# Optimization experiments

Hardware: AMD Instinct MI355X
Metric: run time of the kernel (lower is better)

Reference implementation:

```python
import jax, jax.numpy as jnp
import numpy as np

BETA = 0.25
NUM_CODES = 1024
EMBED_DIM = 256


def setup_inputs() -> dict:
    key = jax.random.key(0)
    k1, k2 = jax.random.split(key)
    z = jax.random.normal(k1, (64, 32, 32, EMBED_DIM), dtype=jnp.float32)
    # torch init: uniform(-1/num_codes, 1/num_codes)
    codebook = jax.random.uniform(k2, (NUM_CODES, EMBED_DIM), dtype=jnp.float32,
                                  minval=-1.0 / NUM_CODES, maxval=1.0 / NUM_CODES)
    return {"z": z, "codebook": codebook}


def reference(z, codebook):
    shape = z.shape
    z_flat = z.reshape(-1, EMBED_DIM)  # [N, D]
    # squared-distance matrix: ||z||^2 + ||c||^2 - 2 z c^T  -> [N, K]
    d = (jnp.sum(z_flat * z_flat, axis=1, keepdims=True)
         + jnp.sum(codebook * codebook, axis=1)
         - 2.0 * jnp.einsum('nd,kd->nk', z_flat, codebook))
    codes = jnp.argmin(d, axis=1)              # [N] int
    quantized = codebook[codes]                # [N, D] gather
    sg = jax.lax.stop_gradient
    cb_loss = jnp.mean((quantized - sg(z_flat)) ** 2)
    cmt_loss = jnp.mean((z_flat - sg(quantized)) ** 2)
    vq_loss = cb_loss + BETA * cmt_loss
    # straight-through estimator
    out = z_flat + sg(quantized - z_flat)
    return out.reshape(shape), codes.reshape(shape[:-1]), vq_loss
```

## Files before the change

### kernel.cpp

```cpp
#include <hip/hip_runtime.h>


#define N_PTS    65536
#define K_CODES  1024
#define DIM      256
#define MARGIN   1.5e-4f
#define WSKIP    4096

#define OUT_VALS  16777216
#define OUT_CODES 65536

typedef __attribute__((ext_vector_type(8))) short short8v;
typedef __attribute__((ext_vector_type(8))) _Float16 half8v;
typedef __attribute__((ext_vector_type(4))) float float4v;

__device__ __forceinline__ int perm_idx(int r, int k) {
  return ((((r >> 4) * 8 + (k >> 5)) * 4 + ((k >> 3) & 3)) * 128) + (r & 15) * 8 + (k & 7);
}

__device__ __forceinline__ short f2h_bits(float x) {
  union { _Float16 h; short s; } u;
  u.h = (_Float16)x;
  return u.s;
}

__device__ __forceinline__ void gload16(const void* g, void* l) {
  __builtin_amdgcn_global_load_lds(
      (const __attribute__((address_space(1))) unsigned*)g,
      (__attribute__((address_space(3))) unsigned*)l, 16, 0, 0);
}

__global__ void prep_cb_kernel(const float* __restrict__ cb,
                               short* __restrict__ cbh_perm,
                               float* __restrict__ Bf,
                               unsigned long long* __restrict__ scratch,
                               unsigned long long* __restrict__ ws0) {
  const int gid = blockIdx.x * 256 + threadIdx.x;
  scratch[gid] = ~0ull;
  if (gid < 512) ws0[gid] = 0ull;
  int r    = blockIdx.x * 4 + (threadIdx.x >> 6);
  int lane = threadIdx.x & 63;
  const float4 v = *(const float4*)(cb + (size_t)r * DIM + lane * 4);
  double s = (double)v.x * v.x + (double)v.y * v.y
           + (double)v.z * v.z + (double)v.w * v.w;
#pragma unroll
  for (int off = 32; off > 0; off >>= 1) s += __shfl_down(s, off);
  if (lane == 0) Bf[r] = (float)s;
  short4 h = make_short4(f2h_bits(v.x * 1024.0f), f2h_bits(v.y * 1024.0f),
                         f2h_bits(v.z * 1024.0f), f2h_bits(v.w * 1024.0f));
  *(short4*)(cbh_perm + perm_idx(r, lane * 4)) = h;
}

__global__ __launch_bounds__(512, 4) void argmin_mfma_kernel(
    const float* __restrict__ z, const float* __restrict__ cb,
    const short* __restrict__ cbh_perm,
    const float* __restrict__ Bf, float* __restrict__ outq,
    float* __restrict__ codes_out,
    int* __restrict__ cnt2, int* __restrict__ cntf,
    unsigned* __restrict__ flag2, int* __restrict__ flagf,
    float* __restrict__ bv2a, float* __restrict__ bvfa,
    double* __restrict__ loss_slots) {
  __shared__ __align__(16) short lbuf[2][2][4096];
  __shared__ float mv1[128][2], mv2[128][2], mv3[128][2];
  __shared__ int   mk1[128][2], mk2[128][2];
  __shared__ float mz[128];
  __shared__ int   scodes[128];
  __shared__ double wls[2];
  const int t    = threadIdx.x;
  const int w    = t >> 6;
  const int l    = t & 63;
  const int quad = l >> 4;
  const int lr   = l & 15;
  const int wp   = w >> 1;
  const int h    = w & 1;
  const int m0   = blockIdx.x * 128;
  const int pbase = m0 + wp * 32;

  {
    const char* src = (const char*)cbh_perm + (size_t)(h * 32) * 8192 + wp * 2048;
    char* dst = (char*)&lbuf[h][0][0] + wp * 2048;
    gload16(src + l * 16, dst + l * 16);
    gload16(src + 1024 + l * 16, dst + 1024 + l * 16);
  }

  half8v ah[2][8];
  float Szrow[2];
#pragma unroll
  for (int a = 0; a < 2; ++a) {
    const float* zrow = z + (size_t)(pbase + a * 16 + lr) * DIM;
    double zs = 0.0;
#pragma unroll
    for (int q = 0; q < 8; ++q) {
      float4 p0 = *(const float4*)(zrow + q * 32 + quad * 8);
      float4 p1 = *(const float4*)(zrow + q * 32 + quad * 8 + 4);
      zs = fma((double)p0.x, (double)p0.x, zs);
      zs = fma((double)p0.y, (double)p0.y, zs);
      zs = fma((double)p0.z, (double)p0.z, zs);
      zs = fma((double)p0.w, (double)p0.w, zs);
      zs = fma((double)p1.x, (double)p1.x, zs);
      zs = fma((double)p1.y, (double)p1.y, zs);
      zs = fma((double)p1.z, (double)p1.z, zs);
      zs = fma((double)p1.w, (double)p1.w, zs);
      half8v hh;
      hh[0] = (_Float16)p0.x; hh[1] = (_Float16)p0.y;
      hh[2] = (_Float16)p0.z; hh[3] = (_Float16)p0.w;
      hh[4] = (_Float16)p1.x; hh[5] = (_Float16)p1.y;
      hh[6] = (_Float16)p1.z; hh[7] = (_Float16)p1.w;
      ah[a][q] = hh;
    }
    zs += __shfl_xor(zs, 16);
    zs += __shfl_xor(zs, 32);
    Szrow[a] = (float)zs;
  }

  float bv[8], sv[8], tv[8]; int bk[8], sk[8];
#pragma unroll
  for (int s = 0; s < 8; ++s) {
    bv[s] = 3.0e38f; sv[s] = 3.0e38f; tv[s] = 3.0e38f; bk[s] = 0; sk[s] = 0;
  }

  __syncthreads();
  int cur = 0;
  for (int it = 0; it < 32; ++it) {
    if (it < 31) {
      const char* src = (const char*)cbh_perm + (size_t)(h * 32 + it + 1) * 8192 + wp * 2048;
      char* dst = (char*)&lbuf[h][cur ^ 1][0] + wp * 2048;
      gload16(src + l * 16, dst + l * 16);
      gload16(src + 1024 + l * 16, dst + 1024 + l * 16);
    }
    const short* bb = &lbuf[h][cur][0];
    float4v acc0 = {0.f, 0.f, 0.f, 0.f};
    float4v acc1 = {0.f, 0.f, 0.f, 0.f};
#pragma unroll
    for (int q = 0; q < 8; ++q) {
      half8v b = *(const half8v*)(bb + q * 512 + quad * 128 + lr * 8);
      acc0 = __builtin_amdgcn_mfma_f32_16x16x32_f16(ah[0][q], b, acc0, 0, 0, 0);
      acc1 = __builtin_amdgcn_mfma_f32_16x16x32_f16(ah[1][q], b, acc1, 0, 0, 0);
    }
    const int k = (h * 32 + it) * 16 + lr;
    const float bkf = Bf[k];
#pragma unroll
    for (int a = 0; a < 2; ++a) {
#pragma unroll
      for (int r = 0; r < 4; ++r) {
        const int s = a * 4 + r;
        float v = fmaf(-0.001953125f, a ? acc1[r] : acc0[r], bkf);
        bool lt1 = v < bv[s];
        bool lt2 = v < sv[s];
        tv[s] = fminf(fmaxf(v, sv[s]), tv[s]);
        sv[s] = fminf(fmaxf(v, bv[s]), sv[s]);
        bv[s] = fminf(v, bv[s]);
        sk[s] = lt1 ? bk[s] : (lt2 ? k : sk[s]);
        bk[s] = lt1 ? k : bk[s];
      }
    }
    __syncthreads();
    cur ^= 1;
  }

#pragma unroll
  for (int mask = 1; mask < 16; mask <<= 1) {
#pragma unroll
    for (int s = 0; s < 8; ++s) {
      float ov  = __shfl_xor(bv[s], mask);
      float os  = __shfl_xor(sv[s], mask);
      float ot  = __shfl_xor(tv[s], mask);
      int   ok  = __shfl_xor(bk[s], mask);
      int   osk = __shfl_xor(sk[s], mask);
      bool win = (ov < bv[s]) || (ov == bv[s] && ok < bk[s]);
      float a1 = win ? ov : bv[s], a2 = win ? os : sv[s], a3 = win ? ot : tv[s];
      int   a1k = win ? ok : bk[s], a2k = win ? osk : sk[s];
      float b1 = win ? bv[s] : ov, b2 = win ? sv[s] : os;
      int   b1k = win ? bk[s] : ok;
      bool s2 = (a2 < b1) || (a2 == b1 && a2k < b1k);
      bv[s] = a1; bk[s] = a1k;
      sv[s] = s2 ? a2 : b1; sk[s] = s2 ? a2k : b1k;
      tv[s] = s2 ? fminf(a3, b1) : fminf(a2, b2);
    }
  }

  if (lr == 0) {
#pragma unroll
    for (int a = 0; a < 2; ++a)
#pragma unroll
      for (int r = 0; r < 4; ++r) {
        int s  = a * 4 + r;
        int pt = wp * 32 + a * 16 + quad * 4 + r;
        mv1[pt][h] = bv[s]; mv2[pt][h] = sv[s]; mv3[pt][h] = tv[s];
        mk1[pt][h] = bk[s]; mk2[pt][h] = sk[s];
      }
  }
  if (h == 0 && quad == 0) {
#pragma unroll
    for (int a = 0; a < 2; ++a)
      mz[wp * 32 + a * 16 + lr] = Szrow[a];
  }
  __syncthreads();

  double ls = 0.0;
  if (t < 128) {
    float a1 = mv1[t][0], a2 = mv2[t][0], a3 = mv3[t][0];
    int   a1k = mk1[t][0], a2k = mk2[t][0];
    float c1 = mv1[t][1], c2 = mv2[t][1], c3 = mv3[t][1];
    int   c1k = mk1[t][1], c2k = mk2[t][1];
    bool win = (c1 < a1) || (c1 == a1 && c1k < a1k);
    float x1 = win ? c1 : a1, x2 = win ? c2 : a2, x3 = win ? c3 : a3;
    int   x1k = win ? c1k : a1k, x2k = win ? c2k : a2k;
    float y1 = win ? a1 : c1, y2 = win ? a2 : c2;
    int   y1k = win ? a1k : c1k;
    bool s2 = (x2 < y1) || (x2 == y1 && x2k < y1k);
    float f2v = s2 ? x2 : y1; int f2k = s2 ? x2k : y1k;
    float f3v = s2 ? fminf(x3, y1) : fminf(x2, y2);
    int n = m0 + t;
    codes_out[n] = (float)x1k;
    scodes[t] = x1k;
    float vrow = mz[t] + x1;
    ls = (double)vrow;
    if (f3v - x1 < MARGIN) {
      int pos = atomicAdd(cntf, 1);
      flagf[pos] = n; bvfa[pos] = vrow;
    } else if (f2v - x1 < MARGIN) {
      int pos = atomicAdd(cnt2, 1);
      flag2[pos] = (unsigned)n | ((unsigned)f2k << 16);
      bv2a[pos] = vrow;
    }
  }
#pragma unroll
  for (int off = 32; off > 0; off >>= 1) ls += __shfl_down(ls, off);
  if (l == 0 && w < 2) wls[w] = ls;
  __syncthreads();

  if (m0 >= WSKIP) {
#pragma unroll
    for (int i = 0; i < 16; ++i) {
      int row = i * 8 + w;
      int c = scodes[row];
      *(float4*)(outq + (size_t)(m0 + row) * DIM + l * 4) =
          *(const float4*)(cb + (size_t)c * DIM + l * 4);
    }
  }
  if (t == 0)
    atomicAdd(&loss_slots[blockIdx.x & 255], wls[0] + wls[1]);
}

__global__ __launch_bounds__(256) void fixup_pair_kernel(
    const float* __restrict__ z, const float* __restrict__ cb,
    const float* __restrict__ Bf, const unsigned* __restrict__ flag2,
    const int* __restrict__ cnt2, const float* __restrict__ bv2a,
    float* __restrict__ codes_out, float* __restrict__ outq,
    double* __restrict__ loss_slots) {
  const int t   = threadIdx.x;
  const int l   = t & 63;
  const int h   = l >> 5;
  const int sub = l & 31;
  const int wid = blockIdx.x * 4 + (t >> 6);
  const int nw  = gridDim.x * 4;
  const int cnt = *cnt2;
  for (int i = wid; i < cnt; i += nw) {
    const unsigned rec = flag2[i];
    const int n  = rec & 0xFFFF;
    const int k2 = rec >> 16;
    const int k1 = (int)codes_out[n];
    const int k  = h ? k2 : k1;
    const float* zr = z + (size_t)n * DIM + sub * 8;
    const float* cr = cb + (size_t)k * DIM + sub * 8;
    const float4 za = *(const float4*)(zr);
    const float4 zb = *(const float4*)(zr + 4);
    const float4 ca = *(const float4*)(cr);
    const float4 cv = *(const float4*)(cr + 4);
    double s = (double)za.x*za.x + (double)za.y*za.y + (double)za.z*za.z + (double)za.w*za.w
             + (double)zb.x*zb.x + (double)zb.y*zb.y + (double)zb.z*zb.z + (double)zb.w*zb.w;
    double d = (double)za.x*ca.x + (double)za.y*ca.y + (double)za.z*ca.z + (double)za.w*ca.w
             + (double)zb.x*cv.x + (double)zb.y*cv.y + (double)zb.z*cv.z + (double)zb.w*cv.w;
#pragma unroll
    for (int m = 1; m < 32; m <<= 1) {
      s += __shfl_xor(s, m);
      d += __shfl_xor(d, m);
    }
    const float Sfl = (float)s;
    const float T1  = Sfl + Bf[k];
    const float v   = T1 - 2.0f * (float)d;
    const float vo  = __shfl_xor(v, 32);
    const int   ko  = __shfl_xor(k, 32);
    const bool keep = (v < vo) || (v == vo && k < ko);
    const float vmin = keep ? v : vo;
    const int   kf   = keep ? k : ko;
    if (l == 0) {
      codes_out[n] = (float)kf;
      atomicAdd(&loss_slots[n & 255], (double)(vmin - bv2a[i]));
    }
    if (kf != k1 && n >= WSKIP)
      *(float4*)(outq + (size_t)n * DIM + l * 4) =
          *(const float4*)(cb + (size_t)kf * DIM + l * 4);
  }
}

__global__ __launch_bounds__(256) void fixup_full_kernel(
    const float* __restrict__ z, const float* __restrict__ cb,
    const float* __restrict__ Bf, const int* __restrict__ flagf,
    const int* __restrict__ cntf, unsigned long long* __restrict__ scratch) {
  __shared__ float vred[4];
  __shared__ int   kred[4];
  const int t = threadIdx.x;
  const int w = t >> 6;
  const int l = t & 63;
  const int cnt = *cntf;
  for (int ib = blockIdx.x; (ib >> 2) < cnt; ib += gridDim.x) {
    const int i = ib >> 2, q = ib & 3;
    const int n = flagf[i];
    const float4 zv = *(const float4*)(z + (size_t)n * DIM + l * 4);
    double s = (double)zv.x*zv.x + (double)zv.y*zv.y
             + (double)zv.z*zv.z + (double)zv.w*zv.w;
#pragma unroll
    for (int off = 32; off > 0; off >>= 1) s += __shfl_xor(s, off);
    const float Sfl = (float)s;
    float bvv = 3.0e38f; int bkk = 0;
    const int kbase = q * 256 + w * 64;
#pragma unroll 4
    for (int k0 = 0; k0 < 64; ++k0) {
      const int k = kbase + k0;
      const float4 cv = *(const float4*)(cb + (size_t)k * DIM + l * 4);
      double d = (double)zv.x*cv.x + (double)zv.y*cv.y
               + (double)zv.z*cv.z + (double)zv.w*cv.w;
#pragma unroll
      for (int off = 32; off > 0; off >>= 1) d += __shfl_xor(d, off);
      float T1 = Sfl + Bf[k];
      float v  = T1 - 2.0f * (float)d;
      if (v < bvv) { bvv = v; bkk = k; }
    }
    __syncthreads();
    if (l == 0) { vred[w] = bvv; kred[w] = bkk; }
    __syncthreads();
    if (t == 0) {
      float fv = vred[0]; int fk = kred[0];
#pragma unroll
      for (int j = 1; j < 4; ++j) {
        float v2 = vred[j]; int kk = kred[j];
        if (v2 < fv || (v2 == fv && kk < fk)) { fv = v2; fk = kk; }
      }
      unsigned long long key =
          ((unsigned long long)__float_as_uint(fv) << 32) | (unsigned)fk;
      atomicMin(&scratch[n], key);
    }
  }
}

__global__ __launch_bounds__(256) void fixup_write_kernel(
    const int* __restrict__ flagf, const int* __restrict__ cntf,
    const unsigned long long* __restrict__ scratch,
    const float* __restrict__ bvfa, const float* __restrict__ cb,
    float* __restrict__ codes_out, float* __restrict__ outq,
    double* __restrict__ loss_slots) {
  const int t = threadIdx.x, l = t & 63;
  const int wid = blockIdx.x * 4 + (t >> 6);
  const int nw  = gridDim.x * 4;
  const int cnt = *cntf;
  for (int i = wid; i < cnt; i += nw) {
    const int n = flagf[i];
    const unsigned long long key = scratch[n];
    const int   fk = (int)(unsigned)(key & 0xFFFFFFFFull);
    const float fv = __uint_as_float((unsigned)(key >> 32));
    const int   k1 = (int)codes_out[n];
    if (l == 0) {
      codes_out[n] = (float)fk;
      atomicAdd(&loss_slots[n & 255], (double)(fv - bvfa[i]));
    }
    if (fk != k1 && n >= WSKIP)
      *(float4*)(outq + (size_t)n * DIM + l * 4) =
          *(const float4*)(cb + (size_t)fk * DIM + l * 4);
  }
}

__global__ void small_gather_kernel(const float* __restrict__ cb,
                                    const float* __restrict__ codes_f,
                                    float* __restrict__ outq) {
  int gid = blockIdx.x * 256 + threadIdx.x;
  int n = gid >> 6, l = gid & 63;
  int c = (int)codes_f[n];
  *(float4*)(outq + (size_t)n * DIM + l * 4) =
      *(const float4*)(cb + (size_t)c * DIM + l * 4);
}

__global__ void finalize_kernel(const double* __restrict__ loss_slots,
                                float* __restrict__ out_loss) {
  const int t = threadIdx.x;
  double s = loss_slots[t];
#pragma unroll
  for (int off = 32; off > 0; off >>= 1) s += __shfl_down(s, off);
  __shared__ double ws[4];
  if ((t & 63) == 0) ws[t >> 6] = s;
  __syncthreads();
  if (t == 0) {
    double tot = ws[0] + ws[1] + ws[2] + ws[3];
    out_loss[0] = (float)(1.25 * tot / (double)(N_PTS * (size_t)DIM));
  }
}

extern "C" void kernel_launch(void* const* d_in, const int* in_sizes, int n_in,
                              void* d_out, int out_size, void* d_ws, size_t ws_size,
                              hipStream_t stream) {
  const float* z  = (const float*)d_in[0];
  const float* cb = (const float*)d_in[1];
  float* out = (float*)d_out;
  double* loss_slots = (double*)d_ws;
  int*      cnt2  = (int*)((char*)d_ws + 2048);
  int*      cntf  = (int*)((char*)d_ws + 2052);
  float*    Bf    = (float*)((char*)d_ws + 4096);
  unsigned* flag2 = (unsigned*)((char*)d_ws + 8192);
  short* cbh_perm = (short*)d_out;
  float* bv2a     = (float*)((char*)d_out + 524288);
  float* bvfa     = (float*)((char*)d_out + 786432);
  unsigned long long* scratch = (unsigned long long*)((char*)d_out + 1048576);
  int*   flagf    = (int*)((char*)d_out + 1572864);

  prep_cb_kernel<<<K_CODES / 4, 256, 0, stream>>>(
      cb, cbh_perm, Bf, scratch, (unsigned long long*)d_ws);
  argmin_mfma_kernel<<<N_PTS / 128, 512, 0, stream>>>(
      z, cb, cbh_perm, Bf, out, out + OUT_VALS, cnt2, cntf, flag2, flagf,
      bv2a, bvfa, loss_slots);
  fixup_pair_kernel<<<1024, 256, 0, stream>>>(
      z, cb, Bf, flag2, cnt2, bv2a, out + OUT_VALS, out, loss_slots);
  fixup_full_kernel<<<2048, 256, 0, stream>>>(z, cb, Bf, flagf, cntf, scratch);
  fixup_write_kernel<<<64, 256, 0, stream>>>(
      flagf, cntf, scratch, bvfa, cb, out + OUT_VALS, out, loss_slots);
  small_gather_kernel<<<WSKIP * 64 / 256, 256, 0, stream>>>(
      cb, out + OUT_VALS, out);
  finalize_kernel<<<1, 256, 0, stream>>>(loss_slots, out + OUT_VALS + OUT_CODES);
}
```

Baseline: 226.1 us.

## Halve argmin block size, pack code indices, merge fixup and finalize kernels

Shrinks the main argmin kernel from 128-point/512-thread blocks to 64-point/256-thread blocks, so there are twice as many smaller blocks. Packs the best and second-best code indices into one 16-bit-pair register to cut register pressure and select work. Rewrites the full fixup so each flagged point is handled by a single block with no atomicMin scratch, which drops the scratch init and the separate write kernel. Folds the loss finalize into the gather kernel, reducing the launch count. The extra fixup work per block and the doubled codebook streaming per point are the tradeoffs.

New measurement: 237.8 us. 1.05x slower.

```diff
diff --git a/kernel.cpp b/kernel.cpp
--- a/kernel.cpp
+++ b/kernel.cpp
@@ -33,10 +33,8 @@
 __global__ void prep_cb_kernel(const float* __restrict__ cb,
                                short* __restrict__ cbh_perm,
                                float* __restrict__ Bf,
-                               unsigned long long* __restrict__ scratch,
                                unsigned long long* __restrict__ ws0) {
   const int gid = blockIdx.x * 256 + threadIdx.x;
-  scratch[gid] = ~0ull;
   if (gid < 512) ws0[gid] = 0ull;
   int r    = blockIdx.x * 4 + (threadIdx.x >> 6);
   int lane = threadIdx.x & 63;
@@ -51,7 +49,7 @@
   *(short4*)(cbh_perm + perm_idx(r, lane * 4)) = h;
 }
 
-__global__ __launch_bounds__(512, 4) void argmin_mfma_kernel(
+__global__ __launch_bounds__(256, 4) void argmin_mfma_kernel(
     const float* __restrict__ z, const float* __restrict__ cb,
     const short* __restrict__ cbh_perm,
     const float* __restrict__ Bf, float* __restrict__ outq,
@@ -61,11 +59,10 @@
     float* __restrict__ bv2a, float* __restrict__ bvfa,
     double* __restrict__ loss_slots) {
   __shared__ __align__(16) short lbuf[2][2][4096];
-  __shared__ float mv1[128][2], mv2[128][2], mv3[128][2];
-  __shared__ int   mk1[128][2], mk2[128][2];
-  __shared__ float mz[128];
-  __shared__ int   scodes[128];
-  __shared__ double wls[2];
+  __shared__ float mv1[64][2], mv2[64][2], mv3[64][2];
+  __shared__ int   mk1[64][2], mk2[64][2];
+  __shared__ float mz[64];
+  __shared__ int   scodes[64];
   const int t    = threadIdx.x;
   const int w    = t >> 6;
   const int l    = t & 63;
@@ -73,14 +70,15 @@
   const int lr   = l & 15;
   const int wp   = w >> 1;
   const int h    = w & 1;
-  const int m0   = blockIdx.x * 128;
+  const int m0   = blockIdx.x * 64;
   const int pbase = m0 + wp * 32;
 
   {
-    const char* src = (const char*)cbh_perm + (size_t)(h * 32) * 8192 + wp * 2048;
-    char* dst = (char*)&lbuf[h][0][0] + wp * 2048;
-    gload16(src + l * 16, dst + l * 16);
-    gload16(src + 1024 + l * 16, dst + 1024 + l * 16);
+    const char* src = (const char*)cbh_perm + (size_t)(h * 32) * 8192 + wp * 4096;
+    char* dst = (char*)&lbuf[h][0][0] + wp * 4096;
+#pragma unroll
+    for (int i = 0; i < 4; ++i)
+      gload16(src + i * 1024 + l * 16, dst + i * 1024 + l * 16);
   }
 
   half8v ah[2][8];
@@ -113,20 +111,21 @@
     Szrow[a] = (float)zs;
   }
 
-  float bv[8], sv[8], tv[8]; int bk[8], sk[8];
+  float bv[8], sv[8], tv[8]; unsigned bksk[8];
 #pragma unroll
   for (int s = 0; s < 8; ++s) {
-    bv[s] = 3.0e38f; sv[s] = 3.0e38f; tv[s] = 3.0e38f; bk[s] = 0; sk[s] = 0;
+    bv[s] = 3.0e38f; sv[s] = 3.0e38f; tv[s] = 3.0e38f; bksk[s] = 0u;
   }
 
   __syncthreads();
   int cur = 0;
   for (int it = 0; it < 32; ++it) {
     if (it < 31) {
-      const char* src = (const char*)cbh_perm + (size_t)(h * 32 + it + 1) * 8192 + wp * 2048;
-      char* dst = (char*)&lbuf[h][cur ^ 1][0] + wp * 2048;
-      gload16(src + l * 16, dst + l * 16);
-      gload16(src + 1024 + l * 16, dst + 1024 + l * 16);
+      const char* src = (const char*)cbh_perm + (size_t)(h * 32 + it + 1) * 8192 + wp * 4096;
+      char* dst = (char*)&lbuf[h][cur ^ 1][0] + wp * 4096;
+#pragma unroll
+      for (int i = 0; i < 4; ++i)
+        gload16(src + i * 1024 + l * 16, dst + i * 1024 + l * 16);
     }
     const short* bb = &lbuf[h][cur][0];
     float4v acc0 = {0.f, 0.f, 0.f, 0.f};
@@ -150,13 +149,18 @@
         tv[s] = fminf(fmaxf(v, sv[s]), tv[s]);
         sv[s] = fminf(fmaxf(v, bv[s]), sv[s]);
         bv[s] = fminf(v, bv[s]);
-        sk[s] = lt1 ? bk[s] : (lt2 ? k : sk[s]);
-        bk[s] = lt1 ? k : bk[s];
+        unsigned u1 = (bksk[s] << 16) | (unsigned)k;
+        unsigned u2 = (bksk[s] & 0xFFFFu) | ((unsigned)k << 16);
+        bksk[s] = lt1 ? u1 : (lt2 ? u2 : bksk[s]);
       }
     }
     __syncthreads();
     cur ^= 1;
   }
+
+  int bk[8], sk[8];
+#pragma unroll
+  for (int s = 0; s < 8; ++s) { bk[s] = bksk[s] & 0xFFFF; sk[s] = bksk[s] >> 16; }
 
 #pragma unroll
   for (int mask = 1; mask < 16; mask <<= 1) {
@@ -191,14 +195,13 @@
       }
   }
   if (h == 0 && quad == 0) {
-#pragma unroll
-    for (int a = 0; a < 2; ++a)
-      mz[wp * 32 + a * 16 + lr] = Szrow[a];
+    mz[wp * 32 + lr]      = Szrow[0];
+    mz[wp * 32 + 16 + lr] = Szrow[1];
   }
   __syncthreads();
 
   double ls = 0.0;
-  if (t < 128) {
+  if (t < 64) {
     float a1 = mv1[t][0], a2 = mv2[t][0], a3 = mv3[t][0];
     int   a1k = mk1[t][0], a2k = mk2[t][0];
     float c1 = mv1[t][1], c2 = mv2[t][1], c3 = mv3[t][1];
@@ -214,33 +217,37 @@
     int n = m0 + t;
     codes_out[n] = (float)x1k;
     scodes[t] = x1k;
-    float vrow = mz[t] + x1;
-    ls = (double)vrow;
+    float vrowv = mz[t] + x1;
+    ls = (double)vrowv;
     if (f3v - x1 < MARGIN) {
       int pos = atomicAdd(cntf, 1);
-      flagf[pos] = n; bvfa[pos] = vrow;
+      flagf[pos] = n; bvfa[pos] = vrowv;
     } else if (f2v - x1 < MARGIN) {
       int pos = atomicAdd(cnt2, 1);
       flag2[pos] = (unsigned)n | ((unsigned)f2k << 16);
-      bv2a[pos] = vrow;
-    }
-  }
-#pragma unroll
-  for (int off = 32; off > 0; off >>= 1) ls += __shfl_down(ls, off);
-  if (l == 0 && w < 2) wls[w] = ls;
+      bv2a[pos] = vrowv;
+    }
+  }
+  if (w == 0) {
+    ls += __shfl_down(ls, 32);
+    ls += __shfl_down(ls, 16);
+    ls += __shfl_down(ls, 8);
+    ls += __shfl_down(ls, 4);
+    ls += __shfl_down(ls, 2);
+    ls += __shfl_down(ls, 1);
+    if (t == 0) atomicAdd(&loss_slots[blockIdx.x & 255], ls);
+  }
   __syncthreads();
 
   if (m0 >= WSKIP) {
 #pragma unroll
     for (int i = 0; i < 16; ++i) {
-      int row = i * 8 + w;
+      int row = i * 4 + w;
       int c = scodes[row];
       *(float4*)(outq + (size_t)(m0 + row) * DIM + l * 4) =
           *(const float4*)(cb + (size_t)c * DIM + l * 4);
     }
   }
-  if (t == 0)
-    atomicAdd(&loss_slots[blockIdx.x & 255], wls[0] + wls[1]);
 }
 
 __global__ __launch_bounds__(256) void fixup_pair_kernel(
@@ -298,15 +305,17 @@
 __global__ __launch_bounds__(256) void fixup_full_kernel(
     const float* __restrict__ z, const float* __restrict__ cb,
     const float* __restrict__ Bf, const int* __restrict__ flagf,
-    const int* __restrict__ cntf, unsigned long long* __restrict__ scratch) {
+    const int* __restrict__ cntf, const float* __restrict__ bvfa,
+    float* __restrict__ codes_out, float* __restrict__ outq,
+    double* __restrict__ loss_slots) {
   __shared__ float vred[4];
   __shared__ int   kred[4];
+  __shared__ int   sfin[2];
   const int t = threadIdx.x;
   const int w = t >> 6;
   const int l = t & 63;
   const int cnt = *cntf;
-  for (int ib = blockIdx.x; (ib >> 2) < cnt; ib += gridDim.x) {
-    const int i = ib >> 2, q = ib & 3;
+  for (int i = blockIdx.x; i < cnt; i += gridDim.x) {
     const int n = flagf[i];
     const float4 zv = *(const float4*)(z + (size_t)n * DIM + l * 4);
     double s = (double)zv.x*zv.x + (double)zv.y*zv.y
@@ -315,9 +324,9 @@
     for (int off = 32; off > 0; off >>= 1) s += __shfl_xor(s, off);
     const float Sfl = (float)s;
     float bvv = 3.0e38f; int bkk = 0;
-    const int kbase = q * 256 + w * 64;
+    const int kbase = w * 256;
 #pragma unroll 4
-    for (int k0 = 0; k0 < 64; ++k0) {
+    for (int k0 = 0; k0 < 256; ++k0) {
       const int k = kbase + k0;
       const float4 cv = *(const float4*)(cb + (size_t)k * DIM + l * 4);
       double d = (double)zv.x*cv.x + (double)zv.y*cv.y
@@ -338,62 +347,40 @@
         float v2 = vred[j]; int kk = kred[j];
         if (v2 < fv || (v2 == fv && kk < fk)) { fv = v2; fk = kk; }
       }
-      unsigned long long key =
-          ((unsigned long long)__float_as_uint(fv) << 32) | (unsigned)fk;
-      atomicMin(&scratch[n], key);
-    }
-  }
-}
-
-__global__ __launch_bounds__(256) void fixup_write_kernel(
-    const int* __restrict__ flagf, const int* __restrict__ cntf,
-    const unsigned long long* __restrict__ scratch,
-    const float* __restrict__ bvfa, const float* __restrict__ cb,
-    float* __restrict__ codes_out, float* __restrict__ outq,
-    double* __restrict__ loss_slots) {
-  const int t = threadIdx.x, l = t & 63;
-  const int wid = blockIdx.x * 4 + (t >> 6);
-  const int nw  = gridDim.x * 4;
-  const int cnt = *cntf;
-  for (int i = wid; i < cnt; i += nw) {
-    const int n = flagf[i];
-    const unsigned long long key = scratch[n];
-    const int   fk = (int)(unsigned)(key & 0xFFFFFFFFull);
-    const float fv = __uint_as_float((unsigned)(key >> 32));
-    const int   k1 = (int)codes_out[n];
-    if (l == 0) {
+      sfin[0] = fk; sfin[1] = (int)codes_out[n];
       codes_out[n] = (float)fk;
       atomicAdd(&loss_slots[n & 255], (double)(fv - bvfa[i]));
     }
-    if (fk != k1 && n >= WSKIP)
-      *(float4*)(outq + (size_t)n * DIM + l * 4) =
-          *(const float4*)(cb + (size_t)fk * DIM + l * 4);
-  }
-}
-
-__global__ void small_gather_kernel(const float* __restrict__ cb,
-                                    const float* __restrict__ codes_f,
-                                    float* __restrict__ outq) {
+    __syncthreads();
+    if (sfin[0] != sfin[1] && n >= WSKIP)
+      outq[(size_t)n * DIM + t] = cb[(size_t)sfin[0] * DIM + t];
+  }
+}
+
+__global__ void gather_finalize_kernel(const float* __restrict__ cb,
+                                       const float* __restrict__ codes_f,
+                                       float* __restrict__ outq,
+                                       const double* __restrict__ loss_slots,
+                                       float* __restrict__ out_loss) {
+  if (blockIdx.x == WSKIP / 4) {
+    const int t = threadIdx.x;
+    double s = loss_slots[t];
+#pragma unroll
+    for (int off = 32; off > 0; off >>= 1) s += __shfl_down(s, off);
+    __shared__ double ws[4];
+    if ((t & 63) == 0) ws[t >> 6] = s;
+    __syncthreads();
+    if (t == 0) {
+      double tot = ws[0] + ws[1] + ws[2] + ws[3];
+      out_loss[0] = (float)(1.25 * tot / (double)(N_PTS * (size_t)DIM));
+    }
+    return;
+  }
   int gid = blockIdx.x * 256 + threadIdx.x;
   int n = gid >> 6, l = gid & 63;
   int c = (int)codes_f[n];
   *(float4*)(outq + (size_t)n * DIM + l * 4) =
       *(const float4*)(cb + (size_t)c * DIM + l * 4);
-}
-
-__global__ void finalize_kernel(const double* __restrict__ loss_slots,
-                                float* __restrict__ out_loss) {
-  const int t = threadIdx.x;
-  double s = loss_slots[t];
-#pragma unroll
-  for (int off = 32; off > 0; off >>= 1) s += __shfl_down(s, off);
-  __shared__ double ws[4];
-  if ((t & 63) == 0) ws[t >> 6] = s;
-  __syncthreads();
-  if (t == 0) {
-    double tot = ws[0] + ws[1] + ws[2] + ws[3];
-    out_loss[0] = (float)(1.25 * tot / (double)(N_PTS * (size_t)DIM));
-  }
 }
 
 extern "C" void kernel_launch(void* const* d_in, const int* in_sizes, int n_in,
@@ -410,20 +397,17 @@
   short* cbh_perm = (short*)d_out;
   float* bv2a     = (float*)((char*)d_out + 524288);
   float* bvfa     = (float*)((char*)d_out + 786432);
-  unsigned long long* scratch = (unsigned long long*)((char*)d_out + 1048576);
   int*   flagf    = (int*)((char*)d_out + 1572864);
 
   prep_cb_kernel<<<K_CODES / 4, 256, 0, stream>>>(
-      cb, cbh_perm, Bf, scratch, (unsigned long long*)d_ws);
-  argmin_mfma_kernel<<<N_PTS / 128, 512, 0, stream>>>(
+      cb, cbh_perm, Bf, (unsigned long long*)d_ws);
+  argmin_mfma_kernel<<<N_PTS / 64, 256, 0, stream>>>(
       z, cb, cbh_perm, Bf, out, out + OUT_VALS, cnt2, cntf, flag2, flagf,
       bv2a, bvfa, loss_slots);
   fixup_pair_kernel<<<1024, 256, 0, stream>>>(
       z, cb, Bf, flag2, cnt2, bv2a, out + OUT_VALS, out, loss_slots);
-  fixup_full_kernel<<<2048, 256, 0, stream>>>(z, cb, Bf, flagf, cntf, scratch);
-  fixup_write_kernel<<<64, 256, 0, stream>>>(
-      flagf, cntf, scratch, bvfa, cb, out + OUT_VALS, out, loss_slots);
-  small_gather_kernel<<<WSKIP * 64 / 256, 256, 0, stream>>>(
-      cb, out + OUT_VALS, out);
-  finalize_kernel<<<1, 256, 0, stream>>>(loss_slots, out + OUT_VALS + OUT_CODES);
-}
+  fixup_full_kernel<<<2048, 256, 0, stream>>>(
+      z, cb, Bf, flagf, cntf, bvfa, out + OUT_VALS, out, loss_slots);
+  gather_finalize_kernel<<<WSKIP / 4 + 1, 256, 0, stream>>>(
+      cb, out + OUT_VALS, out, loss_slots, out + OUT_VALS + OUT_CODES);
+}
```
